# Performance work log

Hardware: AMD Instinct MI355X
Metric: run time of the kernel (lower is better)

Reference implementation:

```python
import jax, jax.numpy as jnp
import numpy as np

B, N, C = 1, 2048, 2048
H, KV, D = 32, 8, 64          # query heads, kv heads, head_dim
G = H // KV                    # groups per kv head
EPS = 1e-6
ROPE_BASE = 10000.0


def rmsnorm(x, w, eps=EPS):
    # normalize over the full last dim (H*D or KV*D), as in the module
    var = jnp.mean(jnp.square(x), axis=-1, keepdims=True)
    return x * jax.lax.rsqrt(var + eps) * w


def rope(x):
    # x: [B, N, h, D]; interleaved-pair rotary embedding (torchtune style)
    b, n, h, d = x.shape
    half = d // 2
    inv_freq = 1.0 / (ROPE_BASE ** (jnp.arange(0, d, 2, dtype=jnp.float32) / d))  # [half]
    ang = jnp.arange(n, dtype=jnp.float32)[:, None] * inv_freq[None, :]           # [N, half]
    cos = jnp.cos(ang)[None, :, None, :]
    sin = jnp.sin(ang)[None, :, None, :]
    xr = x.reshape(b, n, h, half, 2)
    x1, x2 = xr[..., 0], xr[..., 1]
    out = jnp.stack([x1 * cos - x2 * sin, x1 * sin + x2 * cos], axis=-1)
    return out.reshape(b, n, h, d)


def setup_inputs() -> dict:
    key = jax.random.key(0)
    ks = jax.random.split(key, 7)
    s = 0.02
    return {
        "x": jax.random.normal(ks[0], (B, N, C), dtype=jnp.float32),
        "wq": jax.random.normal(ks[1], (H * D, C), dtype=jnp.float32) * s,
        "wk": jax.random.normal(ks[2], (KV * D, C), dtype=jnp.float32) * s,
        "wv": jax.random.normal(ks[3], (KV * D, C), dtype=jnp.float32) * s,
        "wo": jax.random.normal(ks[4], (C, C), dtype=jnp.float32) * s,
        "q_norm_w": 1.0 + 0.01 * jax.random.normal(ks[5], (H * D,), dtype=jnp.float32),
        "k_norm_w": 1.0 + 0.01 * jax.random.normal(ks[6], (KV * D,), dtype=jnp.float32),
    }


def reference(x, wq, wk, wv, wo, q_norm_w, k_norm_w):
    scale = D ** -0.5
    q = jnp.einsum("bnc,oc->bno", x, wq)   # [B,N,H*D]
    k = jnp.einsum("bnc,oc->bno", x, wk)   # [B,N,KV*D]
    v = jnp.einsum("bnc,oc->bno", x, wv)
    q = rmsnorm(q, q_norm_w)               # QK-RMSNorm over flat head dims
    k = rmsnorm(k, k_norm_w)
    q = rope(q.reshape(B, N, H, D))
    k = rope(k.reshape(B, N, KV, D))
    v = v.reshape(B, N, KV, D)
    # GQA: group query heads per kv head, no explicit k/v expand
    qg = q.reshape(B, N, KV, G, D)
    scores = jnp.einsum("bnkgd,bmkd->bkgnm", qg, k) * scale  # [B,KV,G,N,N]
    causal = jnp.tril(jnp.ones((N, N), dtype=bool))
    scores = jnp.where(causal[None, None, None], scores, jnp.finfo(scores.dtype).min)
    probs = jax.nn.softmax(scores, axis=-1)
    out = jnp.einsum("bkgnm,bmkd->bnkgd", probs, v).reshape(B, N, H * D)
    return jnp.einsum("bno,co->bnc", out, wo)
```

## Files before the change

### kernel.cpp

```cpp
#include <hip/hip_runtime.h>

typedef __attribute__((ext_vector_type(8))) short short8;
typedef __attribute__((ext_vector_type(4))) float f32x4;

#define MFMA_BF16 __builtin_amdgcn_mfma_f32_16x16x32_bf16

__device__ __forceinline__ unsigned short f2bf(float f) {
  unsigned u = __builtin_bit_cast(unsigned, f);
  u += 0x7fffu + ((u >> 16) & 1u);
  return (unsigned short)(u >> 16);
}

__global__ __launch_bounds__(256) void f2b5_kernel(const float* __restrict__ x,
                                                   const float* __restrict__ wq,
                                                   const float* __restrict__ wk,
                                                   const float* __restrict__ wv,
                                                   const float* __restrict__ wo,
                                                   unsigned short* __restrict__ xb,
                                                   unsigned short* __restrict__ wb,
                                                   unsigned short* __restrict__ wob) {
  const int b = blockIdx.x;
  const float* src;
  unsigned short* dst;
  int base;
  if (b < 4096)      { src = x;  dst = xb;                base = b; }
  else if (b < 8192) { src = wq; dst = wb;                base = b - 4096; }
  else if (b < 9216) { src = wk; dst = wb + 2048 * 2048;  base = b - 8192; }
  else if (b < 10240){ src = wv; dst = wb + 2560 * 2048;  base = b - 9216; }
  else               { src = wo; dst = wob;               base = b - 10240; }
  const int i = base * 256 + threadIdx.x;
  const float4 v = ((const float4*)src)[i];
  ushort4 o = make_ushort4(f2bf(v.x), f2bf(v.y), f2bf(v.z), f2bf(v.w));
  ((ushort4*)dst)[i] = o;
}

__global__ __launch_bounds__(256) void trig_kernel(float* __restrict__ cosT, float* __restrict__ sinT) {
  int i = blockIdx.x * 256 + threadIdx.x;
  int n = i >> 5, f = i & 31;
  double ang = (double)n * pow(10000.0, -(double)f / 32.0);
  cosT[i] = (float)cos(ang);
  sinT[i] = (float)sin(ang);
}

__global__ __launch_bounds__(256) void add2_kernel(const float* __restrict__ a,
                                                   const float* __restrict__ b,
                                                   float* __restrict__ o) {
  int i = blockIdx.x * 256 + threadIdx.x;
#pragma unroll
  for (int s = 0; s < 2; ++s) {
    const float4 u = ((const float4*)a)[i], v = ((const float4*)b)[i];
    ((float4*)o)[i] = make_float4(u.x + v.x, u.y + v.y, u.z + v.z, u.w + v.w);
    i += 524288;
  }
}

__global__ __launch_bounds__(256) void gemm_bt(const short* __restrict__ A,
                                               const short* __restrict__ B,
                                               float* __restrict__ C,
                                               int M, int N, int K, int KC) {
  __shared__ __align__(16) short As[2][128 * 32];
  __shared__ __align__(16) short Bs[2][128 * 32];
  const int tid = threadIdx.x;
  const int w = tid >> 6, lane = tid & 63;
  const int fr = lane & 15, fs = lane >> 4;
  const size_t brow = (size_t)blockIdx.y * 128, bcol = (size_t)blockIdx.x * 128;
  const int wr = (w >> 1) * 64, wc = (w & 1) * 64;
  const int lr = tid >> 2;
  const int lcS = ((tid & 3) ^ (lr & 3)) * 8;
  const int ks = blockIdx.z * KC;
  C += (size_t)blockIdx.z * ((size_t)M * N);
  const short* ga = A + (brow + lr) * (size_t)K + lcS + ks;
  const short* gb = B + (bcol + lr) * (size_t)K + lcS + ks;
  f32x4 acc[4][4] = {};

  auto stage = [&](int sb, int k0) {
    short* lA = As[sb] + w * 512;
    short* lB = Bs[sb] + w * 512;
    __builtin_amdgcn_global_load_lds((__attribute__((address_space(1))) void*)(ga + k0),
                                     (__attribute__((address_space(3))) void*)(lA), 16, 0, 0);
    __builtin_amdgcn_global_load_lds((__attribute__((address_space(1))) void*)(ga + (size_t)64 * K + k0),
                                     (__attribute__((address_space(3))) void*)(lA + 2048), 16, 0, 0);
    __builtin_amdgcn_global_load_lds((__attribute__((address_space(1))) void*)(gb + k0),
                                     (__attribute__((address_space(3))) void*)(lB), 16, 0, 0);
    __builtin_amdgcn_global_load_lds((__attribute__((address_space(1))) void*)(gb + (size_t)64 * K + k0),
                                     (__attribute__((address_space(3))) void*)(lB + 2048), 16, 0, 0);
  };

  const int nk = KC >> 5;
  stage(0, 0);
  __syncthreads();
  int buf = 0;
  for (int t = 0; t < nk; ++t) {
    if (t + 1 < nk) stage(buf ^ 1, (t + 1) * 32);
    short8 af[4], bfr[4];
#pragma unroll
    for (int m = 0; m < 4; ++m)
      af[m] = *(const short8*)(As[buf] + (wr + m * 16 + fr) * 32 + ((fs ^ (fr & 3)) * 8));
#pragma unroll
    for (int n = 0; n < 4; ++n)
      bfr[n] = *(const short8*)(Bs[buf] + (wc + n * 16 + fr) * 32 + ((fs ^ (fr & 3)) * 8));
#pragma unroll
    for (int m = 0; m < 4; ++m)
#pragma unroll
      for (int n = 0; n < 4; ++n)
        acc[m][n] = MFMA_BF16(af[m], bfr[n], acc[m][n], 0, 0, 0);
    __syncthreads();
    buf ^= 1;
  }
#pragma unroll
  for (int m = 0; m < 4; ++m)
#pragma unroll
    for (int n = 0; n < 4; ++n)
#pragma unroll
      for (int j = 0; j < 4; ++j)
        C[(brow + wr + m * 16 + fs * 4 + j) * (size_t)N + bcol + wc + n * 16 + fr] = acc[m][n][j];
}

__global__ __launch_bounds__(256) void prep_kernel(const float* __restrict__ qkv,
                                                   const float* __restrict__ qw,
                                                   const float* __restrict__ kw,
                                                   const float* __restrict__ cosT,
                                                   const float* __restrict__ sinT,
                                                   short* __restrict__ qb,
                                                   short* __restrict__ kb,
                                                   short* __restrict__ vbt) {
  const int n = blockIdx.x, t = threadIdx.x;
  const int w = t >> 6, lane = t & 63;
  __shared__ float redq[4], redk[4];
  const float* rowA = qkv + (size_t)n * 3072;
  const float* rowB = rowA + 6291456;
  const float* cT = cosT + n * 32;
  const float* sT = sinT + n * 32;
  const float4* r4a = (const float4*)rowA;
  const float4* r4b = (const float4*)rowB;
  float4 a0 = r4a[t * 2], a1 = r4b[t * 2];
  float4 b0 = r4a[t * 2 + 1], b1 = r4b[t * 2 + 1];
  float4 a = make_float4(a0.x + a1.x, a0.y + a1.y, a0.z + a1.z, a0.w + a1.w);
  float4 b = make_float4(b0.x + b1.x, b0.y + b1.y, b0.z + b1.z, b0.w + b1.w);
  float ss = a.x*a.x + a.y*a.y + a.z*a.z + a.w*a.w + b.x*b.x + b.y*b.y + b.z*b.z + b.w*b.w;
#pragma unroll
  for (int off = 32; off > 0; off >>= 1) ss += __shfl_xor(ss, off);
  if (lane == 0) redq[w] = ss;
  __syncthreads();
  float rsq = rsqrtf((redq[0] + redq[1] + redq[2] + redq[3]) * (1.0f / 2048.f) + 1e-6f)
              * 0.125f * 1.44269504088896f;
  const int base = t * 8;
  float y[8] = {a.x, a.y, a.z, a.w, b.x, b.y, b.z, b.w};
#pragma unroll
  for (int e = 0; e < 8; ++e) y[e] *= rsq * qw[base + e];
  short8 ov;
  const int dbase = base & 63;
#pragma unroll
  for (int p = 0; p < 4; ++p) {
    float c = cT[(dbase >> 1) + p], s = sT[(dbase >> 1) + p];
    float x1 = y[2 * p], x2 = y[2 * p + 1];
    ov[2 * p]     = (short)f2bf(x1 * c - x2 * s);
    ov[2 * p + 1] = (short)f2bf(x1 * s + x2 * c);
  }
  const int h = base >> 6;
  *(short8*)(qb + ((size_t)h * 2048 + n) * 64 + dbase) = ov;
  const int ki = t * 2;
  float2 k0 = *(const float2*)(rowA + 2048 + ki);
  float2 k1 = *(const float2*)(rowB + 2048 + ki);
  float2 kv2 = make_float2(k0.x + k1.x, k0.y + k1.y);
  float ssk = kv2.x * kv2.x + kv2.y * kv2.y;
#pragma unroll
  for (int off = 32; off > 0; off >>= 1) ssk += __shfl_xor(ssk, off);
  if (lane == 0) redk[w] = ssk;
  __syncthreads();
  float rsk = rsqrtf((redk[0] + redk[1] + redk[2] + redk[3]) * (1.0f / 512.f) + 1e-6f);
  float z0 = kv2.x * rsk * kw[ki], z1 = kv2.y * rsk * kw[ki + 1];
  const int kd = ki & 63, kvh = ki >> 6;
  {
    float c = cT[kd >> 1], s = sT[kd >> 1];
    ushort2 o2 = make_ushort2(f2bf(z0 * c - z1 * s), f2bf(z0 * s + z1 * c));
    *(ushort2*)(kb + ((size_t)kvh * 2048 + n) * 64 + kd) = o2;
  }
  float2 v0 = *(const float2*)(rowA + 2560 + ki);
  float2 v1 = *(const float2*)(rowB + 2560 + ki);
  vbt[((size_t)kvh * 64 + kd) * 2048 + n]       = (short)f2bf(v0.x + v1.x);
  vbt[((size_t)kvh * 64 + kd + 1) * 2048 + n]   = (short)f2bf(v0.y + v1.y);
}

__global__ __launch_bounds__(256, 4) void attn_kernel(const short* __restrict__ qb,
                                                      const short* __restrict__ kb,
                                                      const short* __restrict__ vbt,
                                                      short* __restrict__ ab) {
  const int bid = blockIdx.x;
  const int h = bid & 31;
  const int qblk = 31 - (bid >> 5);
  const int kvh = h >> 2;
  const int tid = threadIdx.x;
  const int w = tid >> 6, lane = tid & 63;
  const int fr = lane & 15, fs = lane >> 4;
  const int q0w = qblk * 64 + w * 16;
  __shared__ __align__(16) short Ks[2][64][64];
  __shared__ __align__(16) short Vs[2][64][64];
  __shared__ __align__(16) short Ps[4][16][64];
  const short* Kb = kb + (size_t)kvh * 2048 * 64;
  const short* Vb = vbt + (size_t)kvh * 64 * 2048;
  short8 qf[2];
  {
    const short* qrow = qb + ((size_t)h * 2048 + q0w + fr) * 64;
    qf[0] = *(const short8*)(qrow + fs * 8);
    qf[1] = *(const short8*)(qrow + 32 + fs * 8);
  }
  short8 ones8;
#pragma unroll
  for (int e = 0; e < 8; ++e) ones8[e] = (short)0x3F80;
  f32x4 accO[4] = {};
  f32x4 lacc = {};
  float mrow[4] = {-1e30f, -1e30f, -1e30f, -1e30f};

  const int rS = lane >> 3;
  const int cS = (lane & 7) ^ rS;
  auto stage = [&](int sb, int kv0s) {
#pragma unroll
    for (int i = 0; i < 2; ++i) {
      int r = i * 32 + w * 8 + rS;
      __builtin_amdgcn_global_load_lds(
          (__attribute__((address_space(1))) void*)(Kb + (size_t)(kv0s + r) * 64 + cS * 8),
          (__attribute__((address_space(3))) void*)(&Ks[sb][0][0] + i * 2048 + w * 512), 16, 0, 0);
      __builtin_amdgcn_global_load_lds(
          (__attribute__((address_space(1))) void*)(Vb + (size_t)r * 2048 + kv0s + cS * 8),
          (__attribute__((address_space(3))) void*)(&Vs[sb][0][0] + i * 2048 + w * 512), 16, 0, 0);
    }
  };

  const int ntiles = qblk + 1;
  int buf = 0;
  stage(0, 0);
  __syncthreads();
  for (int t = 0; t < ntiles; ++t) {
    const int kv0 = t * 64;
    if (t + 1 < ntiles) stage(buf ^ 1, (t + 1) * 64);
    const short* KsB = &Ks[buf][0][0];
    const short* VsB = &Vs[buf][0][0];
    const int sw = (fr & 7);
    f32x4 sc[4];
#pragma unroll
    for (int ct = 0; ct < 4; ++ct) {
      const int rk = ct * 16 + fr;
      short8 kf0 = *(const short8*)(KsB + rk * 64 + ((fs ^ sw) * 8));
      short8 kf1 = *(const short8*)(KsB + rk * 64 + (((4 + fs) ^ sw) * 8));
      f32x4 a = {};
      a = MFMA_BF16(qf[0], kf0, a, 0, 0, 0);
      a = MFMA_BF16(qf[1], kf1, a, 0, 0, 0);
      sc[ct] = a;
    }
    if (t == qblk) {
#pragma unroll
      for (int ct = 0; ct < 4; ++ct) {
        const int col = kv0 + ct * 16 + fr;
#pragma unroll
        for (int j = 0; j < 4; ++j)
          if (col > q0w + fs * 4 + j) sc[ct][j] = -1e30f;
      }
    }
    float pmax[4];
    int defer_ok = 1;
#pragma unroll
    for (int j = 0; j < 4; ++j) {
      float v = fmaxf(fmaxf(sc[0][j], sc[1][j]), fmaxf(sc[2][j], sc[3][j]));
#pragma unroll
      for (int off = 1; off < 16; off <<= 1) v = fmaxf(v, __shfl_xor(v, off));
      pmax[j] = v;
      defer_ok &= (v - mrow[j] <= 8.0f);
    }
    if (!__all(defer_ok)) {
      float resc[4];
#pragma unroll
      for (int j = 0; j < 4; ++j) {
        float mn = fmaxf(mrow[j], pmax[j]);
        resc[j] = exp2f(mrow[j] - mn);
        mrow[j] = mn;
        lacc[j] *= resc[j];
      }
#pragma unroll
      for (int dt = 0; dt < 4; ++dt)
#pragma unroll
        for (int j = 0; j < 4; ++j) accO[dt][j] *= resc[j];
    }
#pragma unroll
    for (int ct = 0; ct < 4; ++ct)
#pragma unroll
      for (int j = 0; j < 4; ++j) {
        const int r = fs * 4 + j;
        Ps[w][r][(ct * 16 + fr) ^ ((r & 7) << 3)] = (short)f2bf(exp2f(sc[ct][j] - mrow[j]));
      }
    short8 pa[2];
#pragma unroll
    for (int s = 0; s < 2; ++s)
      pa[s] = *(const short8*)(&Ps[w][fr][((s * 4 + fs) ^ (fr & 7)) * 8]);
    lacc = MFMA_BF16(pa[0], ones8, lacc, 0, 0, 0);
    lacc = MFMA_BF16(pa[1], ones8, lacc, 0, 0, 0);
#pragma unroll
    for (int dt = 0; dt < 4; ++dt) {
      const int rv = dt * 16 + fr;
      short8 vf0 = *(const short8*)(VsB + rv * 64 + ((fs ^ sw) * 8));
      short8 vf1 = *(const short8*)(VsB + rv * 64 + (((4 + fs) ^ sw) * 8));
      accO[dt] = MFMA_BF16(pa[0], vf0, accO[dt], 0, 0, 0);
      accO[dt] = MFMA_BF16(pa[1], vf1, accO[dt], 0, 0, 0);
    }
    __syncthreads();
    buf ^= 1;
  }
  float invl[4];
#pragma unroll
  for (int j = 0; j < 4; ++j) invl[j] = 1.0f / lacc[j];
#pragma unroll
  for (int dt = 0; dt < 4; ++dt)
#pragma unroll
    for (int j = 0; j < 4; ++j)
      ab[(size_t)(q0w + fs * 4 + j) * 2048 + h * 64 + dt * 16 + fr] =
          (short)f2bf(accO[dt][j] * invl[j]);
}

extern "C" void kernel_launch(void* const* d_in, const int* in_sizes, int n_in,
                              void* d_out, int out_size, void* d_ws, size_t ws_size,
                              hipStream_t stream) {
  const float* x  = (const float*)d_in[0];
  const float* wq = (const float*)d_in[1];
  const float* wk = (const float*)d_in[2];
  const float* wv = (const float*)d_in[3];
  const float* wo = (const float*)d_in[4];
  const float* qw = (const float*)d_in[5];
  const float* kw = (const float*)d_in[6];
  float* out = (float*)d_out;
  char* ws = (char*)d_ws;
  short* xb    = (short*)(ws + 0);
  short* wb    = (short*)(ws + 8388608);
  short* wob   = (short*)(ws + 20971520);
  float* qkvfA = (float*)(ws + 29360128);
  float* qkvfB = (float*)(ws + 54525952);
  short* qb    = (short*)(ws + 79691776);
  short* kb    = (short*)(ws + 88080384);
  short* vbt   = (short*)(ws + 90177536);
  float* cosT  = (float*)(ws + 92274688);
  float* sinT  = (float*)(ws + 92536832);
  short* ab = xb;
  float* po0 = qkvfA;
  float* po1 = qkvfA + 4194304;
  (void)qkvfB; (void)ws_size;

  f2b5_kernel<<<14336, 256, 0, stream>>>(x, wq, wk, wv, wo,
                                         (unsigned short*)xb, (unsigned short*)wb,
                                         (unsigned short*)wob);
  trig_kernel<<<256, 256, 0, stream>>>(cosT, sinT);
  gemm_bt<<<dim3(24, 16, 2), 256, 0, stream>>>(xb, wb, qkvfA, 2048, 3072, 2048, 1024);
  prep_kernel<<<2048, 256, 0, stream>>>(qkvfA, qw, kw, cosT, sinT, qb, kb, vbt);
  attn_kernel<<<1024, 256, 0, stream>>>(qb, kb, vbt, ab);
  gemm_bt<<<dim3(16, 16, 2), 256, 0, stream>>>(ab, wob, po0, 2048, 2048, 2048, 1024);
  add2_kernel<<<2048, 256, 0, stream>>>(po0, po1, out);
}
```

Baseline: 166.8 us.

## Pair low and high causal query blocks per attention workgroup to balance load

Each attention workgroup now processes two query blocks (p and 31-p) of the same head, so every block does the same number of KV tiles and each staged K/V tile feeds both query blocks. The grid is halved to 512 blocks and launch bounds drop to 2 waves per SIMD because register use roughly doubles. s_setprio is raised around the PV MFMA section. The aim is to remove causal load imbalance and halve K/V reloads, at the cost of lower occupancy and fewer blocks to spread across CUs.

```diff
diff --git a/kernel.cpp b/kernel.cpp
--- a/kernel.cpp
+++ b/kernel.cpp
@@ -182,35 +182,41 @@
   vbt[((size_t)kvh * 64 + kd + 1) * 2048 + n]   = (short)f2bf(v0.y + v1.y);
 }
 
-__global__ __launch_bounds__(256, 4) void attn_kernel(const short* __restrict__ qb,
+__global__ __launch_bounds__(256, 2) void attn_kernel(const short* __restrict__ qb,
                                                       const short* __restrict__ kb,
                                                       const short* __restrict__ vbt,
                                                       short* __restrict__ ab) {
   const int bid = blockIdx.x;
   const int h = bid & 31;
-  const int qblk = 31 - (bid >> 5);
+  const int p = bid >> 5;
+  const int lo = p, hi = 31 - p;
   const int kvh = h >> 2;
   const int tid = threadIdx.x;
   const int w = tid >> 6, lane = tid & 63;
   const int fr = lane & 15, fs = lane >> 4;
-  const int q0w = qblk * 64 + w * 16;
+  const int q0lo = lo * 64 + w * 16;
+  const int q0hi = hi * 64 + w * 16;
   __shared__ __align__(16) short Ks[2][64][64];
   __shared__ __align__(16) short Vs[2][64][64];
-  __shared__ __align__(16) short Ps[4][16][64];
+  __shared__ __align__(16) short Ps[4][2][16][64];
   const short* Kb = kb + (size_t)kvh * 2048 * 64;
   const short* Vb = vbt + (size_t)kvh * 64 * 2048;
-  short8 qf[2];
+  short8 qfH[2], qfL[2];
   {
-    const short* qrow = qb + ((size_t)h * 2048 + q0w + fr) * 64;
-    qf[0] = *(const short8*)(qrow + fs * 8);
-    qf[1] = *(const short8*)(qrow + 32 + fs * 8);
+    const short* qrowH = qb + ((size_t)h * 2048 + q0hi + fr) * 64;
+    const short* qrowL = qb + ((size_t)h * 2048 + q0lo + fr) * 64;
+    qfH[0] = *(const short8*)(qrowH + fs * 8);
+    qfH[1] = *(const short8*)(qrowH + 32 + fs * 8);
+    qfL[0] = *(const short8*)(qrowL + fs * 8);
+    qfL[1] = *(const short8*)(qrowL + 32 + fs * 8);
   }
   short8 ones8;
 #pragma unroll
   for (int e = 0; e < 8; ++e) ones8[e] = (short)0x3F80;
-  f32x4 accO[4] = {};
-  f32x4 lacc = {};
-  float mrow[4] = {-1e30f, -1e30f, -1e30f, -1e30f};
+  f32x4 accH[4] = {}, accL[4] = {};
+  f32x4 laccH = {}, laccL = {};
+  float mrowH[4] = {-1e30f, -1e30f, -1e30f, -1e30f};
+  float mrowL[4] = {-1e30f, -1e30f, -1e30f, -1e30f};
 
   const int rS = lane >> 3;
   const int cS = (lane & 7) ^ rS;
@@ -227,7 +233,7 @@
     }
   };
 
-  const int ntiles = qblk + 1;
+  const int ntiles = 32 - p;
   int buf = 0;
   stage(0, 0);
   __syncthreads();
@@ -237,83 +243,98 @@
     const short* KsB = &Ks[buf][0][0];
     const short* VsB = &Vs[buf][0][0];
     const int sw = (fr & 7);
-    f32x4 sc[4];
-#pragma unroll
-    for (int ct = 0; ct < 4; ++ct) {
-      const int rk = ct * 16 + fr;
-      short8 kf0 = *(const short8*)(KsB + rk * 64 + ((fs ^ sw) * 8));
-      short8 kf1 = *(const short8*)(KsB + rk * 64 + (((4 + fs) ^ sw) * 8));
-      f32x4 a = {};
-      a = MFMA_BF16(qf[0], kf0, a, 0, 0, 0);
-      a = MFMA_BF16(qf[1], kf1, a, 0, 0, 0);
-      sc[ct] = a;
-    }
-    if (t == qblk) {
+
+    auto proc = [&](const short8 (&qf)[2], f32x4 (&accO)[4], f32x4& lacc, float (&mrow)[4],
+                    short (*PsG)[64], int q0, bool domask) {
+      f32x4 sc[4];
 #pragma unroll
       for (int ct = 0; ct < 4; ++ct) {
-        const int col = kv0 + ct * 16 + fr;
-#pragma unroll
-        for (int j = 0; j < 4; ++j)
-          if (col > q0w + fs * 4 + j) sc[ct][j] = -1e30f;
-      }
-    }
-    float pmax[4];
-    int defer_ok = 1;
-#pragma unroll
-    for (int j = 0; j < 4; ++j) {
-      float v = fmaxf(fmaxf(sc[0][j], sc[1][j]), fmaxf(sc[2][j], sc[3][j]));
-#pragma unroll
-      for (int off = 1; off < 16; off <<= 1) v = fmaxf(v, __shfl_xor(v, off));
-      pmax[j] = v;
-      defer_ok &= (v - mrow[j] <= 8.0f);
-    }
-    if (!__all(defer_ok)) {
-      float resc[4];
+        const int rk = ct * 16 + fr;
+        short8 kf0 = *(const short8*)(KsB + rk * 64 + ((fs ^ sw) * 8));
+        short8 kf1 = *(const short8*)(KsB + rk * 64 + (((4 + fs) ^ sw) * 8));
+        f32x4 a = {};
+        a = MFMA_BF16(qf[0], kf0, a, 0, 0, 0);
+        a = MFMA_BF16(qf[1], kf1, a, 0, 0, 0);
+        sc[ct] = a;
+      }
+      if (domask) {
+#pragma unroll
+        for (int ct = 0; ct < 4; ++ct) {
+          const int col = kv0 + ct * 16 + fr;
+#pragma unroll
+          for (int j = 0; j < 4; ++j)
+            if (col > q0 + fs * 4 + j) sc[ct][j] = -1e30f;
+        }
+      }
+      float pmax[4];
+      int defer_ok = 1;
 #pragma unroll
       for (int j = 0; j < 4; ++j) {
-        float mn = fmaxf(mrow[j], pmax[j]);
-        resc[j] = exp2f(mrow[j] - mn);
-        mrow[j] = mn;
-        lacc[j] *= resc[j];
-      }
-#pragma unroll
-      for (int dt = 0; dt < 4; ++dt)
-#pragma unroll
-        for (int j = 0; j < 4; ++j) accO[dt][j] *= resc[j];
-    }
-#pragma unroll
-    for (int ct = 0; ct < 4; ++ct)
-#pragma unroll
-      for (int j = 0; j < 4; ++j) {
-        const int r = fs * 4 + j;
-        Ps[w][r][(ct * 16 + fr) ^ ((r & 7) << 3)] = (short)f2bf(exp2f(sc[ct][j] - mrow[j]));
-      }
-    short8 pa[2];
-#pragma unroll
-    for (int s = 0; s < 2; ++s)
-      pa[s] = *(const short8*)(&Ps[w][fr][((s * 4 + fs) ^ (fr & 7)) * 8]);
-    lacc = MFMA_BF16(pa[0], ones8, lacc, 0, 0, 0);
-    lacc = MFMA_BF16(pa[1], ones8, lacc, 0, 0, 0);
-#pragma unroll
-    for (int dt = 0; dt < 4; ++dt) {
-      const int rv = dt * 16 + fr;
-      short8 vf0 = *(const short8*)(VsB + rv * 64 + ((fs ^ sw) * 8));
-      short8 vf1 = *(const short8*)(VsB + rv * 64 + (((4 + fs) ^ sw) * 8));
-      accO[dt] = MFMA_BF16(pa[0], vf0, accO[dt], 0, 0, 0);
-      accO[dt] = MFMA_BF16(pa[1], vf1, accO[dt], 0, 0, 0);
-    }
+        float v = fmaxf(fmaxf(sc[0][j], sc[1][j]), fmaxf(sc[2][j], sc[3][j]));
+#pragma unroll
+        for (int off = 1; off < 16; off <<= 1) v = fmaxf(v, __shfl_xor(v, off));
+        pmax[j] = v;
+        defer_ok &= (v - mrow[j] <= 8.0f);
+      }
+      if (!__all(defer_ok)) {
+        float resc[4];
+#pragma unroll
+        for (int j = 0; j < 4; ++j) {
+          float mn = fmaxf(mrow[j], pmax[j]);
+          resc[j] = exp2f(mrow[j] - mn);
+          mrow[j] = mn;
+          lacc[j] *= resc[j];
+        }
+#pragma unroll
+        for (int dt = 0; dt < 4; ++dt)
+#pragma unroll
+          for (int j = 0; j < 4; ++j) accO[dt][j] *= resc[j];
+      }
+#pragma unroll
+      for (int ct = 0; ct < 4; ++ct)
+#pragma unroll
+        for (int j = 0; j < 4; ++j) {
+          const int r = fs * 4 + j;
+          PsG[r][(ct * 16 + fr) ^ ((r & 7) << 3)] = (short)f2bf(exp2f(sc[ct][j] - mrow[j]));
+        }
+      short8 pa[2];
+#pragma unroll
+      for (int s = 0; s < 2; ++s)
+        pa[s] = *(const short8*)(&PsG[fr][((s * 4 + fs) ^ (fr & 7)) * 8]);
+      __builtin_amdgcn_s_setprio(1);
+      lacc = MFMA_BF16(pa[0], ones8, lacc, 0, 0, 0);
+      lacc = MFMA_BF16(pa[1], ones8, lacc, 0, 0, 0);
+#pragma unroll
+      for (int dt = 0; dt < 4; ++dt) {
+        const int rv = dt * 16 + fr;
+        short8 vf0 = *(const short8*)(VsB + rv * 64 + ((fs ^ sw) * 8));
+        short8 vf1 = *(const short8*)(VsB + rv * 64 + (((4 + fs) ^ sw) * 8));
+        accO[dt] = MFMA_BF16(pa[0], vf0, accO[dt], 0, 0, 0);
+        accO[dt] = MFMA_BF16(pa[1], vf1, accO[dt], 0, 0, 0);
+      }
+      __builtin_amdgcn_s_setprio(0);
+    };
+
+    proc(qfH, accH, laccH, mrowH, Ps[w][0], q0hi, t == ntiles - 1);
+    if (t <= lo) proc(qfL, accL, laccL, mrowL, Ps[w][1], q0lo, t == lo);
     __syncthreads();
     buf ^= 1;
   }
-  float invl[4];
-#pragma unroll
-  for (int j = 0; j < 4; ++j) invl[j] = 1.0f / lacc[j];
-#pragma unroll
-  for (int dt = 0; dt < 4; ++dt)
-#pragma unroll
-    for (int j = 0; j < 4; ++j)
-      ab[(size_t)(q0w + fs * 4 + j) * 2048 + h * 64 + dt * 16 + fr] =
-          (short)f2bf(accO[dt][j] * invl[j]);
+#pragma unroll
+  for (int g = 0; g < 2; ++g) {
+    const f32x4* accO = g ? accL : accH;
+    const f32x4& lacc = g ? laccL : laccH;
+    const int q0 = g ? q0lo : q0hi;
+    float invl[4];
+#pragma unroll
+    for (int j = 0; j < 4; ++j) invl[j] = 1.0f / lacc[j];
+#pragma unroll
+    for (int dt = 0; dt < 4; ++dt)
+#pragma unroll
+      for (int j = 0; j < 4; ++j)
+        ab[(size_t)(q0 + fs * 4 + j) * 2048 + h * 64 + dt * 16 + fr] =
+            (short)f2bf(accO[dt][j] * invl[j]);
+  }
 }
 
 extern "C" void kernel_launch(void* const* d_in, const int* in_sizes, int n_in,
@@ -349,7 +370,7 @@
   trig_kernel<<<256, 256, 0, stream>>>(cosT, sinT);
   gemm_bt<<<dim3(24, 16, 2), 256, 0, stream>>>(xb, wb, qkvfA, 2048, 3072, 2048, 1024);
   prep_kernel<<<2048, 256, 0, stream>>>(qkvfA, qw, kw, cosT, sinT, qb, kb, vbt);
-  attn_kernel<<<1024, 256, 0, stream>>>(qb, kb, vbt, ab);
+  attn_kernel<<<512, 256, 0, stream>>>(qb, kb, vbt, ab);
   gemm_bt<<<dim3(16, 16, 2), 256, 0, stream>>>(ab, wob, po0, 2048, 2048, 2048, 1024);
   add2_kernel<<<2048, 256, 0, stream>>>(po0, po1, out);
 }
```

Measured after the change: 166.8 us. No clear change (-0.1%).

## Transpose attention MFMA operands, drop LDS K/V staging, load K/V from global directly

Applied to the files above, without the earlier changes.

The attention kernel no longer stages K and V tiles through double-buffered LDS with __syncthreads. Each wave now reads its K/V fragments straight from global memory (relying on cache reuse) and swaps MFMA operand order, so each lane owns one query row. This turns the row max into a two-step shuffle and lets the running max and rescale become scalars per lane. It also adds packed bf16 conversion via v_cvt_pk_bf16_f32, vectorized P and output stores, and s_setprio around the MFMA block. The cost is more global/L2 traffic for K/V, since the 4 waves in a block each load the same tiles independently and there is no explicit prefetch.

```diff
diff --git a/kernel.cpp b/kernel.cpp
--- a/kernel.cpp
+++ b/kernel.cpp
@@ -9,6 +9,12 @@
   unsigned u = __builtin_bit_cast(unsigned, f);
   u += 0x7fffu + ((u >> 16) & 1u);
   return (unsigned short)(u >> 16);
+}
+
+__device__ __forceinline__ unsigned cvtpk(float a, float b) {
+  unsigned r;
+  asm("v_cvt_pk_bf16_f32 %0, %1, %2" : "=v"(r) : "v"(a), "v"(b));
+  return r;
 }
 
 __global__ __launch_bounds__(256) void f2b5_kernel(const float* __restrict__ x,
@@ -194,14 +200,13 @@
   const int w = tid >> 6, lane = tid & 63;
   const int fr = lane & 15, fs = lane >> 4;
   const int q0w = qblk * 64 + w * 16;
-  __shared__ __align__(16) short Ks[2][64][64];
-  __shared__ __align__(16) short Vs[2][64][64];
+  const int q_lane = q0w + fr;
   __shared__ __align__(16) short Ps[4][16][64];
   const short* Kb = kb + (size_t)kvh * 2048 * 64;
   const short* Vb = vbt + (size_t)kvh * 64 * 2048;
   short8 qf[2];
   {
-    const short* qrow = qb + ((size_t)h * 2048 + q0w + fr) * 64;
+    const short* qrow = qb + ((size_t)h * 2048 + q_lane) * 64;
     qf[0] = *(const short8*)(qrow + fs * 8);
     qf[1] = *(const short8*)(qrow + 32 + fs * 8);
   }
@@ -210,110 +215,90 @@
   for (int e = 0; e < 8; ++e) ones8[e] = (short)0x3F80;
   f32x4 accO[4] = {};
   f32x4 lacc = {};
-  float mrow[4] = {-1e30f, -1e30f, -1e30f, -1e30f};
-
-  const int rS = lane >> 3;
-  const int cS = (lane & 7) ^ rS;
-  auto stage = [&](int sb, int kv0s) {
-#pragma unroll
-    for (int i = 0; i < 2; ++i) {
-      int r = i * 32 + w * 8 + rS;
-      __builtin_amdgcn_global_load_lds(
-          (__attribute__((address_space(1))) void*)(Kb + (size_t)(kv0s + r) * 64 + cS * 8),
-          (__attribute__((address_space(3))) void*)(&Ks[sb][0][0] + i * 2048 + w * 512), 16, 0, 0);
-      __builtin_amdgcn_global_load_lds(
-          (__attribute__((address_space(1))) void*)(Vb + (size_t)r * 2048 + kv0s + cS * 8),
-          (__attribute__((address_space(3))) void*)(&Vs[sb][0][0] + i * 2048 + w * 512), 16, 0, 0);
-    }
-  };
-
-  const int ntiles = qblk + 1;
-  int buf = 0;
-  stage(0, 0);
-  __syncthreads();
-  for (int t = 0; t < ntiles; ++t) {
+  float m = -1e30f;
+  short* prow = &Ps[w][fr][0];
+  const int swz = (fr & 7) << 1;
+
+  for (int t = 0; t <= qblk; ++t) {
     const int kv0 = t * 64;
-    if (t + 1 < ntiles) stage(buf ^ 1, (t + 1) * 64);
-    const short* KsB = &Ks[buf][0][0];
-    const short* VsB = &Vs[buf][0][0];
-    const int sw = (fr & 7);
+    short8 kf[4][2];
+#pragma unroll
+    for (int ct = 0; ct < 4; ++ct) {
+      const short* kr = Kb + (size_t)(kv0 + ct * 16 + fr) * 64;
+      kf[ct][0] = *(const short8*)(kr + fs * 8);
+      kf[ct][1] = *(const short8*)(kr + 32 + fs * 8);
+    }
     f32x4 sc[4];
 #pragma unroll
     for (int ct = 0; ct < 4; ++ct) {
-      const int rk = ct * 16 + fr;
-      short8 kf0 = *(const short8*)(KsB + rk * 64 + ((fs ^ sw) * 8));
-      short8 kf1 = *(const short8*)(KsB + rk * 64 + (((4 + fs) ^ sw) * 8));
       f32x4 a = {};
-      a = MFMA_BF16(qf[0], kf0, a, 0, 0, 0);
-      a = MFMA_BF16(qf[1], kf1, a, 0, 0, 0);
+      a = MFMA_BF16(kf[ct][0], qf[0], a, 0, 0, 0);
+      a = MFMA_BF16(kf[ct][1], qf[1], a, 0, 0, 0);
       sc[ct] = a;
     }
+    short8 vf[4][2];
+#pragma unroll
+    for (int dt = 0; dt < 4; ++dt) {
+      const short* vr = Vb + (size_t)(dt * 16 + fr) * 2048 + kv0;
+      vf[dt][0] = *(const short8*)(vr + fs * 8);
+      vf[dt][1] = *(const short8*)(vr + 32 + fs * 8);
+    }
     if (t == qblk) {
 #pragma unroll
       for (int ct = 0; ct < 4; ++ct) {
-        const int col = kv0 + ct * 16 + fr;
+        const int kvb = kv0 + ct * 16 + fs * 4;
 #pragma unroll
         for (int j = 0; j < 4; ++j)
-          if (col > q0w + fs * 4 + j) sc[ct][j] = -1e30f;
+          if (kvb + j > q_lane) sc[ct][j] = -1e30f;
       }
     }
-    float pmax[4];
-    int defer_ok = 1;
-#pragma unroll
-    for (int j = 0; j < 4; ++j) {
-      float v = fmaxf(fmaxf(sc[0][j], sc[1][j]), fmaxf(sc[2][j], sc[3][j]));
-#pragma unroll
-      for (int off = 1; off < 16; off <<= 1) v = fmaxf(v, __shfl_xor(v, off));
-      pmax[j] = v;
-      defer_ok &= (v - mrow[j] <= 8.0f);
-    }
-    if (!__all(defer_ok)) {
-      float resc[4];
-#pragma unroll
-      for (int j = 0; j < 4; ++j) {
-        float mn = fmaxf(mrow[j], pmax[j]);
-        resc[j] = exp2f(mrow[j] - mn);
-        mrow[j] = mn;
-        lacc[j] *= resc[j];
-      }
+    float v01 = fmaxf(fmaxf(sc[0][0], sc[0][1]), fmaxf(sc[0][2], sc[0][3]));
+    float v1 = fmaxf(fmaxf(sc[1][0], sc[1][1]), fmaxf(sc[1][2], sc[1][3]));
+    float v2 = fmaxf(fmaxf(sc[2][0], sc[2][1]), fmaxf(sc[2][2], sc[2][3]));
+    float v3 = fmaxf(fmaxf(sc[3][0], sc[3][1]), fmaxf(sc[3][2], sc[3][3]));
+    float vmax = fmaxf(fmaxf(v01, v1), fmaxf(v2, v3));
+    vmax = fmaxf(vmax, __shfl_xor(vmax, 16));
+    vmax = fmaxf(vmax, __shfl_xor(vmax, 32));
+    if (!__all(vmax - m <= 8.0f)) {
+      float mn = fmaxf(m, vmax);
+      float resc = exp2f(m - mn);
+      m = mn;
+      lacc *= resc;
 #pragma unroll
       for (int dt = 0; dt < 4; ++dt)
 #pragma unroll
-        for (int j = 0; j < 4; ++j) accO[dt][j] *= resc[j];
-    }
-#pragma unroll
-    for (int ct = 0; ct < 4; ++ct)
-#pragma unroll
-      for (int j = 0; j < 4; ++j) {
-        const int r = fs * 4 + j;
-        Ps[w][r][(ct * 16 + fr) ^ ((r & 7) << 3)] = (short)f2bf(exp2f(sc[ct][j] - mrow[j]));
-      }
+        for (int j = 0; j < 4; ++j) accO[dt][j] *= resc;
+    }
+#pragma unroll
+    for (int ct = 0; ct < 4; ++ct) {
+      uint2 pk;
+      pk.x = cvtpk(exp2f(sc[ct][0] - m), exp2f(sc[ct][1] - m));
+      pk.y = cvtpk(exp2f(sc[ct][2] - m), exp2f(sc[ct][3] - m));
+      *(uint2*)(prow + (((ct * 4 + fs) ^ swz) * 4)) = pk;
+    }
     short8 pa[2];
 #pragma unroll
     for (int s = 0; s < 2; ++s)
-      pa[s] = *(const short8*)(&Ps[w][fr][((s * 4 + fs) ^ (fr & 7)) * 8]);
-    lacc = MFMA_BF16(pa[0], ones8, lacc, 0, 0, 0);
-    lacc = MFMA_BF16(pa[1], ones8, lacc, 0, 0, 0);
+      pa[s] = *(const short8*)(prow + (((s * 8 + fs * 2) ^ swz) * 4));
+    __builtin_amdgcn_s_setprio(1);
+    lacc = MFMA_BF16(ones8, pa[0], lacc, 0, 0, 0);
+    lacc = MFMA_BF16(ones8, pa[1], lacc, 0, 0, 0);
 #pragma unroll
     for (int dt = 0; dt < 4; ++dt) {
-      const int rv = dt * 16 + fr;
-      short8 vf0 = *(const short8*)(VsB + rv * 64 + ((fs ^ sw) * 8));
-      short8 vf1 = *(const short8*)(VsB + rv * 64 + (((4 + fs) ^ sw) * 8));
-      accO[dt] = MFMA_BF16(pa[0], vf0, accO[dt], 0, 0, 0);
-      accO[dt] = MFMA_BF16(pa[1], vf1, accO[dt], 0, 0, 0);
-    }
-    __syncthreads();
-    buf ^= 1;
-  }
-  float invl[4];
-#pragma unroll
-  for (int j = 0; j < 4; ++j) invl[j] = 1.0f / lacc[j];
-#pragma unroll
-  for (int dt = 0; dt < 4; ++dt)
-#pragma unroll
-    for (int j = 0; j < 4; ++j)
-      ab[(size_t)(q0w + fs * 4 + j) * 2048 + h * 64 + dt * 16 + fr] =
-          (short)f2bf(accO[dt][j] * invl[j]);
+      accO[dt] = MFMA_BF16(vf[dt][0], pa[0], accO[dt], 0, 0, 0);
+      accO[dt] = MFMA_BF16(vf[dt][1], pa[1], accO[dt], 0, 0, 0);
+    }
+    __builtin_amdgcn_s_setprio(0);
+  }
+  const float inv = 1.0f / lacc[0];
+  short* orow = ab + (size_t)q_lane * 2048 + h * 64;
+#pragma unroll
+  for (int dt = 0; dt < 4; ++dt) {
+    uint2 o;
+    o.x = cvtpk(accO[dt][0] * inv, accO[dt][1] * inv);
+    o.y = cvtpk(accO[dt][2] * inv, accO[dt][3] * inv);
+    *(uint2*)(orow + dt * 16 + fs * 4) = o;
+  }
 }
 
 extern "C" void kernel_launch(void* const* d_in, const int* in_sizes, int n_in,
```

New measurement: 253.0 us. 51.7% more time.
